# Kernel tuning notes

Measured on AMD Instinct MI355X. Metric: run time of the kernel, lower is better.

## Reference

```python
import jax, jax.numpy as jnp
import numpy as np

EMB = 1024
HEADS = 16
HEAD_DIM = EMB // HEADS
B, S = 4, 2048


def setup_inputs() -> dict:
    key = jax.random.key(0)
    ks = jax.random.split(key, 9)
    sc = 1.0 / np.sqrt(EMB)
    x = jax.random.normal(ks[0], (B, S, EMB), dtype=jnp.float32)
    Wq = jax.random.normal(ks[1], (EMB, EMB), dtype=jnp.float32) * sc
    bq = jax.random.normal(ks[2], (EMB,), dtype=jnp.float32) * 0.02
    Wk = jax.random.normal(ks[3], (EMB, EMB), dtype=jnp.float32) * sc
    bk = jax.random.normal(ks[4], (EMB,), dtype=jnp.float32) * 0.02
    Wv = jax.random.normal(ks[5], (EMB, EMB), dtype=jnp.float32) * sc
    bv = jax.random.normal(ks[6], (EMB,), dtype=jnp.float32) * 0.02
    Wo = jax.random.normal(ks[7], (EMB, EMB), dtype=jnp.float32) * sc
    bo = jax.random.normal(ks[8], (EMB,), dtype=jnp.float32) * 0.02
    # causal mask: 1 where allowed (lower triangular), 0 elsewhere
    causal_mask = jnp.tril(jnp.ones((S, S), dtype=jnp.int32))[None, None]
    return {"x": x, "Wq": Wq, "bq": bq, "Wk": Wk, "bk": bk,
            "Wv": Wv, "bv": bv, "Wo": Wo, "bo": bo,
            "causal_mask": causal_mask}


def reference(x, Wq, bq, Wk, bk, Wv, bv, Wo, bo, causal_mask):
    bs, seq, _ = x.shape
    # nn.Linear: x @ W.T + b; then view [bs, seq, H, hd] and transpose to [bs, H, seq, hd]
    def proj(W, b):
        return (x @ W.T + b).reshape(bs, seq, HEADS, HEAD_DIM).transpose(0, 2, 1, 3)
    q, k, v = proj(Wq, bq), proj(Wk, bk), proj(Wv, bv)
    scale = 1.0 / np.sqrt(HEAD_DIM).astype(np.float32)
    dots = jnp.einsum('bhqd,bhkd->bhqk', q, k) * scale  # [B, H, S, S]
    dots = jnp.where(causal_mask == 0, -jnp.inf, dots)
    attn = jax.nn.softmax(dots, axis=-1)
    out = jnp.einsum('bhqk,bhkd->bhqd', attn, v)  # [B, H, S, hd]
    out = out.transpose(0, 2, 1, 3).reshape(bs, seq, EMB)
    return out @ Wo.T + bo
```

## Files before the change

kernel.cpp:

```cpp
#include <hip/hip_runtime.h>
#include <hip/hip_bf16.h>

typedef __attribute__((ext_vector_type(8))) short short8;
typedef __attribute__((ext_vector_type(4))) float floatx4;

#define B_    4
#define S_    2048
#define EMB_  1024
#define NH_   16
#define HD_   64

#if __has_builtin(__builtin_amdgcn_exp2f)
#define EXP2F(x) __builtin_amdgcn_exp2f(x)
#else
#define EXP2F(x) exp2f(x)
#endif

__device__ __forceinline__ void async_cp16(const void* g, void* l) {
  __builtin_amdgcn_global_load_lds(
      (const __attribute__((address_space(1))) unsigned int*)g,
      (__attribute__((address_space(3))) unsigned int*)l, 16, 0, 0);
}

__device__ __forceinline__ ushort4 cvt4(const float4 f) {
  __bf16 t[4] = {(__bf16)f.x, (__bf16)f.y, (__bf16)f.z, (__bf16)f.w};
  return *(const ushort4*)t;
}

__global__ __launch_bounds__(256)
void cvt_kernel(const float* __restrict__ x,
                const float* __restrict__ wq, const float* __restrict__ wk,
                const float* __restrict__ wv, const float* __restrict__ wo,
                const float* __restrict__ bq, const float* __restrict__ bk,
                const float* __restrict__ bv,
                __bf16* __restrict__ xb, __bf16* __restrict__ Wcat,
                __bf16* __restrict__ Wob, float* __restrict__ bcat)
{
  const int NX4 = 2097152;
  const int NW4 = 262144;
  int g = blockIdx.x * 256 + threadIdx.x;
  if (g < NX4) {
    *(ushort4*)(xb + (size_t)g * 4) = cvt4(*(const float4*)(x + (size_t)g * 4));
    return;
  }
  g -= NX4;
  if (g < 3 * NW4) {
    const float* src = (g < NW4) ? wq : (g < 2 * NW4) ? wk : wv;
    const int gg = (g < NW4) ? g : (g < 2 * NW4) ? g - NW4 : g - 2 * NW4;
    *(ushort4*)(Wcat + (size_t)g * 4) = cvt4(*(const float4*)(src + (size_t)gg * 4));
    return;
  }
  g -= 3 * NW4;
  if (g < NW4) {
    *(ushort4*)(Wob + (size_t)g * 4) = cvt4(*(const float4*)(wo + (size_t)g * 4));
    return;
  }
  g -= NW4;
  if (g < 768) {
    const float* src = (g < 256) ? bq : (g < 512) ? bk : bv;
    *(float4*)(bcat + (size_t)g * 4) = *(const float4*)(src + (size_t)(g & 255) * 4);
  }
}

__global__ __launch_bounds__(256)
void gemm_qkv_kernel(const __bf16* __restrict__ A, const __bf16* __restrict__ W,
                     const float* __restrict__ bcat,
                     __bf16* __restrict__ Qb, __bf16* __restrict__ Kb,
                     __bf16* __restrict__ Vb)
{
  __shared__ __attribute__((aligned(16))) __bf16 As[128 * 32];
  __shared__ __attribute__((aligned(16))) __bf16 Ws[128 * 32];
  const int tid  = threadIdx.x;
  const int wave = tid >> 6, lane = tid & 63;
  const int l15  = lane & 15, quad = lane >> 4;
  const int wm   = wave >> 1, wn = wave & 1;
  const int bm   = blockIdx.y * 128;
  const int bn   = blockIdx.x * 128;
  const int widx = bn >> 10;
  const float QS = 0.180336880f;

  floatx4 acc[4][4];
#pragma unroll
  for (int i = 0; i < 4; ++i)
#pragma unroll
    for (int j = 0; j < 4; ++j) acc[i][j] = (floatx4){0.f, 0.f, 0.f, 0.f};

  const int srow = tid >> 2;
  const int scol = (tid & 3) << 3;
  const __bf16* Ag = A + (size_t)(bm + srow) * 1024 + scol;
  const __bf16* Wg = W + (size_t)(bn + srow) * 1024 + scol;
  __bf16* AsD = As + tid * 8;
  __bf16* WsD = Ws + tid * 8;

  for (int k0 = 0; k0 < 1024; k0 += 32) {
    __syncthreads();
    async_cp16(Ag + k0,             AsD);
    async_cp16(Ag + k0 + 64 * 1024, AsD + 2048);
    async_cp16(Wg + k0,             WsD);
    async_cp16(Wg + k0 + 64 * 1024, WsD + 2048);
    __syncthreads();
    short8 af[4], wf[4];
#pragma unroll
    for (int mi = 0; mi < 4; ++mi)
      af[mi] = *(const short8*)(As + ((wm * 64 + mi * 16 + l15) << 5) + (quad << 3));
#pragma unroll
    for (int ni = 0; ni < 4; ++ni)
      wf[ni] = *(const short8*)(Ws + ((wn * 64 + ni * 16 + l15) << 5) + (quad << 3));
#pragma unroll
    for (int mi = 0; mi < 4; ++mi)
#pragma unroll
      for (int ni = 0; ni < 4; ++ni)
        acc[mi][ni] = __builtin_amdgcn_mfma_f32_16x16x32_bf16(af[mi], wf[ni], acc[mi][ni], 0, 0, 0);
  }

#pragma unroll
  for (int ni = 0; ni < 4; ++ni) {
    const int n  = bn + wn * 64 + ni * 16 + l15;
    const float bvb = bcat[n];
    const int np = n & 1023;
    const int h = np >> 6, d = np & 63;
#pragma unroll
    for (int mi = 0; mi < 4; ++mi) {
      const int m0 = bm + wm * 64 + mi * 16 + quad * 4;
      const int b = m0 >> 11, s0 = m0 & 2047;
      floatx4 v = acc[mi][ni];
      if (widx == 0) {
        const size_t base = (size_t)(b * 16 + h) * (S_ * 64) + d;
#pragma unroll
        for (int r = 0; r < 4; ++r)
          Qb[base + (size_t)(s0 + r) * 64] = (__bf16)((v[r] + bvb) * QS);
      } else if (widx == 1) {
        const size_t base = (size_t)(b * 16 + h) * (S_ * 64) + d;
#pragma unroll
        for (int r = 0; r < 4; ++r)
          Kb[base + (size_t)(s0 + r) * 64] = (__bf16)(v[r] + bvb);
      } else {
        const size_t base = ((size_t)(b * 16 + h) * 64 + d) * S_ + s0;
        union { ushort4 u4; unsigned short u[4]; } pk;
#pragma unroll
        for (int r = 0; r < 4; ++r) {
          __bf16 hv = (__bf16)(v[r] + bvb);
          pk.u[r] = *(unsigned short*)&hv;
        }
        *(ushort4*)(Vb + base) = pk.u4;
      }
    }
  }
}

__device__ __forceinline__ void softmax_update(
    floatx4* s, float& mrun, float& lsum, floatx4* oacc,
    __bf16* psbase, const int l15, const int quad)
{
  float t0 = fmaxf(fmaxf(s[0][0], s[0][1]), fmaxf(s[0][2], s[0][3]));
  float t1 = fmaxf(fmaxf(s[1][0], s[1][1]), fmaxf(s[1][2], s[1][3]));
  float t2 = fmaxf(fmaxf(s[2][0], s[2][1]), fmaxf(s[2][2], s[2][3]));
  float t3 = fmaxf(fmaxf(s[3][0], s[3][1]), fmaxf(s[3][2], s[3][3]));
  float tmax = fmaxf(fmaxf(t0, t1), fmaxf(t2, t3));
  tmax = fmaxf(tmax, __shfl_xor(tmax, 16));
  tmax = fmaxf(tmax, __shfl_xor(tmax, 32));

  const float mold = mrun;
  if (!__all(tmax <= mold + 8.0f)) {
    const float mnew = fmaxf(mold, tmax);
    const float alpha = EXP2F(mold - mnew);
#pragma unroll
    for (int ni = 0; ni < 4; ++ni)
#pragma unroll
      for (int r = 0; r < 4; ++r) oacc[ni][r] *= alpha;
    lsum *= alpha;
    mrun = mnew;
  }
  const float m = mrun;
  float psum = 0.f;
#pragma unroll
  for (int ni = 0; ni < 4; ++ni) {
    float4 p;
    p.x = EXP2F(s[ni][0] - m);
    p.y = EXP2F(s[ni][1] - m);
    p.z = EXP2F(s[ni][2] - m);
    p.w = EXP2F(s[ni][3] - m);
    psum += (p.x + p.y) + (p.z + p.w);
    *(ushort4*)(psbase + l15 * 72 + ni * 16 + quad * 4) = cvt4(p);
  }
  lsum += psum;
}

__global__ __launch_bounds__(256, 3)
void attn_kernel(__bf16* __restrict__ Q, const __bf16* __restrict__ K,
                 const __bf16* __restrict__ Vt)
{
  __shared__ __attribute__((aligned(16))) __bf16 Ks[64 * 72];
  __shared__ __attribute__((aligned(16))) __bf16 Vs[64 * 72];
  __shared__ __attribute__((aligned(16))) __bf16 Ps[4][2][16 * 72];

  const int tid  = threadIdx.x;
  const int wave = tid >> 6, lane = tid & 63;
  const int l15  = lane & 15, quad = lane >> 4;
  const int qtA  = blockIdx.x, bh = blockIdx.y;
  const size_t hb = (size_t)bh * (S_ * 64);
  const float MASKV = -1.0e30f;

  const int srow = tid >> 3;
  const int scol = (tid & 7) << 3;

  const int qtS = qtA;
  const int qtB = 31 - qtA;
  const int myqS = qtS * 64 + wave * 16 + l15;
  const int myqB = qtB * 64 + wave * 16 + l15;

  short8 aqS[2], aqB[2];
#pragma unroll
  for (int kk = 0; kk < 2; ++kk) {
    aqS[kk] = *(const short8*)(Q + hb + (size_t)myqS * 64 + kk * 32 + quad * 8);
    aqB[kk] = *(const short8*)(Q + hb + (size_t)myqB * 64 + kk * 32 + quad * 8);
  }

  floatx4 oaccS[4], oaccB[4];
#pragma unroll
  for (int j = 0; j < 4; ++j) {
    oaccS[j] = (floatx4){0.f, 0.f, 0.f, 0.f};
    oaccB[j] = (floatx4){0.f, 0.f, 0.f, 0.f};
  }
  float lsumS = 0.f, lsumB = 0.f;
  float mrunS = MASKV, mrunB = MASKV;

  uint4 kreg0, kreg1, vreg0, vreg1;
  {
    const __bf16* kp = K  + hb + (size_t)srow * 64 + scol;
    const __bf16* vp = Vt + hb + (size_t)srow * S_ + scol;
    kreg0 = *(const uint4*)kp;
    kreg1 = *(const uint4*)(kp + 32 * 64);
    vreg0 = *(const uint4*)vp;
    vreg1 = *(const uint4*)(vp + (size_t)32 * S_);
  }

  for (int kt = 0; kt <= qtB; ++kt) {
    const bool haveS = (kt <= qtS);

    __syncthreads();
    *(uint4*)(&Ks[srow * 72 + scol])        = kreg0;
    *(uint4*)(&Ks[(srow + 32) * 72 + scol]) = kreg1;
    *(uint4*)(&Vs[srow * 72 + scol])        = vreg0;
    *(uint4*)(&Vs[(srow + 32) * 72 + scol]) = vreg1;
    __syncthreads();

    if (kt < qtB) {
      const __bf16* kp = K  + hb + (size_t)((kt + 1) * 64 + srow) * 64 + scol;
      const __bf16* vp = Vt + hb + (size_t)srow * S_ + (kt + 1) * 64 + scol;
      kreg0 = *(const uint4*)kp;
      kreg1 = *(const uint4*)(kp + 32 * 64);
      vreg0 = *(const uint4*)vp;
      vreg1 = *(const uint4*)(vp + (size_t)32 * S_);
    }

    floatx4 sS[4], sB[4];
#pragma unroll
    for (int j = 0; j < 4; ++j) {
      sS[j] = (floatx4){0.f, 0.f, 0.f, 0.f};
      sB[j] = (floatx4){0.f, 0.f, 0.f, 0.f};
    }
#pragma unroll
    for (int kk = 0; kk < 2; ++kk) {
      short8 bk[4];
#pragma unroll
      for (int ni = 0; ni < 4; ++ni)
        bk[ni] = *(const short8*)(&Ks[(ni * 16 + l15) * 72 + kk * 32 + quad * 8]);
#pragma unroll
      for (int ni = 0; ni < 4; ++ni)
        sB[ni] = __builtin_amdgcn_mfma_f32_16x16x32_bf16(bk[ni], aqB[kk], sB[ni], 0, 0, 0);
      if (haveS) {
#pragma unroll
        for (int ni = 0; ni < 4; ++ni)
          sS[ni] = __builtin_amdgcn_mfma_f32_16x16x32_bf16(bk[ni], aqS[kk], sS[ni], 0, 0, 0);
      }
    }

    if (kt == qtB) {
      const int kb = kt * 64 + quad * 4;
#pragma unroll
      for (int ni = 0; ni < 4; ++ni)
#pragma unroll
        for (int r = 0; r < 4; ++r)
          if (kb + ni * 16 + r > myqB) sB[ni][r] = MASKV;
    }
    if (haveS) {
      if (kt == qtS) {
        const int kb = kt * 64 + quad * 4;
#pragma unroll
        for (int ni = 0; ni < 4; ++ni)
#pragma unroll
          for (int r = 0; r < 4; ++r)
            if (kb + ni * 16 + r > myqS) sS[ni][r] = MASKV;
      }
      softmax_update(sS, mrunS, lsumS, oaccS, &Ps[wave][0][0], l15, quad);
    }
    softmax_update(sB, mrunB, lsumB, oaccB, &Ps[wave][1][0], l15, quad);

    asm volatile("s_waitcnt lgkmcnt(0)" ::: "memory");
    __builtin_amdgcn_sched_barrier(0);

#pragma unroll
    for (int kk = 0; kk < 2; ++kk) {
      short8 bv[4];
#pragma unroll
      for (int ni = 0; ni < 4; ++ni)
        bv[ni] = *(const short8*)(&Vs[(ni * 16 + l15) * 72 + kk * 32 + quad * 8]);
      const short8 pfB = *(const short8*)(&Ps[wave][1][l15 * 72 + kk * 32 + quad * 8]);
#pragma unroll
      for (int ni = 0; ni < 4; ++ni)
        oaccB[ni] = __builtin_amdgcn_mfma_f32_16x16x32_bf16(bv[ni], pfB, oaccB[ni], 0, 0, 0);
      if (haveS) {
        const short8 pfS = *(const short8*)(&Ps[wave][0][l15 * 72 + kk * 32 + quad * 8]);
#pragma unroll
        for (int ni = 0; ni < 4; ++ni)
          oaccS[ni] = __builtin_amdgcn_mfma_f32_16x16x32_bf16(bv[ni], pfS, oaccS[ni], 0, 0, 0);
      }
    }
  }

  {
    float l = lsumS;
    l += __shfl_xor(l, 16);
    l += __shfl_xor(l, 32);
    const float inv = 1.0f / fmaxf(l, 1e-20f);
    const size_t rowb = hb + (size_t)myqS * 64;
#pragma unroll
    for (int ni = 0; ni < 4; ++ni) {
      float4 o;
      o.x = oaccS[ni][0] * inv;
      o.y = oaccS[ni][1] * inv;
      o.z = oaccS[ni][2] * inv;
      o.w = oaccS[ni][3] * inv;
      *(ushort4*)(Q + rowb + ni * 16 + quad * 4) = cvt4(o);
    }
  }
  {
    float l = lsumB;
    l += __shfl_xor(l, 16);
    l += __shfl_xor(l, 32);
    const float inv = 1.0f / fmaxf(l, 1e-20f);
    const size_t rowb = hb + (size_t)myqB * 64;
#pragma unroll
    for (int ni = 0; ni < 4; ++ni) {
      float4 o;
      o.x = oaccB[ni][0] * inv;
      o.y = oaccB[ni][1] * inv;
      o.z = oaccB[ni][2] * inv;
      o.w = oaccB[ni][3] * inv;
      *(ushort4*)(Q + rowb + ni * 16 + quad * 4) = cvt4(o);
    }
  }
}

__global__ __launch_bounds__(256)
void gemm_o_kernel(const __bf16* __restrict__ A, const __bf16* __restrict__ W,
                   const float* __restrict__ bias, float* __restrict__ out)
{
  __shared__ __attribute__((aligned(16))) __bf16 As[128 * 32];
  __shared__ __attribute__((aligned(16))) __bf16 Ws[128 * 32];
  const int tid  = threadIdx.x;
  const int wave = tid >> 6, lane = tid & 63;
  const int l15  = lane & 15, quad = lane >> 4;
  const int wm   = wave >> 1, wn = wave & 1;
  const int bm   = blockIdx.y * 128;
  const int bn   = blockIdx.x * 128;

  floatx4 acc[4][4];
#pragma unroll
  for (int i = 0; i < 4; ++i)
#pragma unroll
    for (int j = 0; j < 4; ++j) acc[i][j] = (floatx4){0.f, 0.f, 0.f, 0.f};

  const int srow = tid >> 2;
  const int scol = (tid & 3) << 3;
  const __bf16* Wg = W + (size_t)(bn + srow) * 1024 + scol;
  const int bb = bm >> 11;
  const int ss = (bm & 2047) + srow;
  __bf16* AsD = As + tid * 8;
  __bf16* WsD = Ws + tid * 8;

  for (int k0 = 0; k0 < 1024; k0 += 32) {
    const int c = k0 + scol, h = c >> 6, dd = c & 63;
    const __bf16* pa0 = A + (((size_t)(bb * 16 + h) * S_) + ss) * 64 + dd;
    __syncthreads();
    async_cp16(pa0,           AsD);
    async_cp16(pa0 + 64 * 64, AsD + 2048);
    async_cp16(Wg + k0,             WsD);
    async_cp16(Wg + k0 + 64 * 1024, WsD + 2048);
    __syncthreads();

    short8 af[4], wf[4];
#pragma unroll
    for (int mi = 0; mi < 4; ++mi)
      af[mi] = *(const short8*)(As + ((wm * 64 + mi * 16 + l15) << 5) + (quad << 3));
#pragma unroll
    for (int ni = 0; ni < 4; ++ni)
      wf[ni] = *(const short8*)(Ws + ((wn * 64 + ni * 16 + l15) << 5) + (quad << 3));
#pragma unroll
    for (int mi = 0; mi < 4; ++mi)
#pragma unroll
      for (int ni = 0; ni < 4; ++ni)
        acc[mi][ni] = __builtin_amdgcn_mfma_f32_16x16x32_bf16(af[mi], wf[ni], acc[mi][ni], 0, 0, 0);
  }

#pragma unroll
  for (int ni = 0; ni < 4; ++ni) {
    const int n = bn + wn * 64 + ni * 16 + l15;
    const float bvb = bias[n];
#pragma unroll
    for (int mi = 0; mi < 4; ++mi) {
      const int m0 = bm + wm * 64 + mi * 16 + quad * 4;
      floatx4 v = acc[mi][ni];
#pragma unroll
      for (int r = 0; r < 4; ++r)
        out[(size_t)(m0 + r) * 1024 + n] = v[r] + bvb;
    }
  }
}

extern "C" void kernel_launch(void* const* d_in, const int* in_sizes, int n_in,
                              void* d_out, int out_size, void* d_ws, size_t ws_size,
                              hipStream_t stream) {
  const float* x  = (const float*)d_in[0];
  const float* Wq = (const float*)d_in[1];
  const float* bq = (const float*)d_in[2];
  const float* Wk = (const float*)d_in[3];
  const float* bk = (const float*)d_in[4];
  const float* Wv = (const float*)d_in[5];
  const float* bv = (const float*)d_in[6];
  const float* Wo = (const float*)d_in[7];
  const float* bo = (const float*)d_in[8];

  const size_t BUF = (size_t)B_ * NH_ * S_ * HD_;
  __bf16* ws   = (__bf16*)d_ws;
  __bf16* xb   = ws;
  __bf16* Wcat = ws + 8388608;
  __bf16* Wob  = ws + 11534336;
  __bf16* Qb   = ws + 12582912;
  float*  bcat = (float*)(ws + 20971520);
  __bf16* Kb   = (__bf16*)d_out;
  __bf16* Vb   = (__bf16*)d_out + BUF;

  dim3 blk(256);
  cvt_kernel<<<12291, blk, 0, stream>>>(x, Wq, Wk, Wv, Wo, bq, bk, bv,
                                        xb, Wcat, Wob, bcat);
  gemm_qkv_kernel<<<dim3(24, 64), blk, 0, stream>>>(xb, Wcat, bcat, Qb, Kb, Vb);
  attn_kernel<<<dim3(16, 64), blk, 0, stream>>>(Qb, Kb, Vb);
  gemm_o_kernel<<<dim3(8, 64), blk, 0, stream>>>(Qb, Wob, bo, (float*)d_out);
}
```

Baseline: 287.2 us.

## Use 128-row query tiles per block with two 16-row groups per wave

Each attention block now handles a 128-row query tile: every wave owns 32 query rows, split into two 16-row sub-blocks, and each K/V tile loaded into LDS is reused for twice as many queries. Causal load balancing pairs tile qtA with tile 15-qtA, which are processed one after the other instead of together. The grid is halved to 8x64 blocks and the occupancy hint drops from 3 to 2 blocks per CU. The aim is to cut K/V global loads and LDS staging per query. In exchange the kernel has fewer blocks, lower occupancy and more registers per wave, and each pair of tiles now runs sequentially with its own K/V loop.

Result: faster. 274.9 us (-4.3%).

```diff
diff --git a/kernel.cpp b/kernel.cpp
--- a/kernel.cpp
+++ b/kernel.cpp
@@ -186,7 +186,7 @@
   lsum += psum;
 }
 
-__global__ __launch_bounds__(256, 3)
+__global__ __launch_bounds__(256, 2)
 void attn_kernel(__bf16* __restrict__ Q, const __bf16* __restrict__ K,
                  const __bf16* __restrict__ Vt)
 {
@@ -204,151 +204,150 @@
   const int srow = tid >> 3;
   const int scol = (tid & 7) << 3;
 
-  const int qtS = qtA;
-  const int qtB = 31 - qtA;
-  const int myqS = qtS * 64 + wave * 16 + l15;
-  const int myqB = qtB * 64 + wave * 16 + l15;
-
-  short8 aqS[2], aqB[2];
-#pragma unroll
-  for (int kk = 0; kk < 2; ++kk) {
-    aqS[kk] = *(const short8*)(Q + hb + (size_t)myqS * 64 + kk * 32 + quad * 8);
-    aqB[kk] = *(const short8*)(Q + hb + (size_t)myqB * 64 + kk * 32 + quad * 8);
-  }
-
-  floatx4 oaccS[4], oaccB[4];
-#pragma unroll
-  for (int j = 0; j < 4; ++j) {
-    oaccS[j] = (floatx4){0.f, 0.f, 0.f, 0.f};
-    oaccB[j] = (floatx4){0.f, 0.f, 0.f, 0.f};
-  }
-  float lsumS = 0.f, lsumB = 0.f;
-  float mrunS = MASKV, mrunB = MASKV;
-
-  uint4 kreg0, kreg1, vreg0, vreg1;
-  {
-    const __bf16* kp = K  + hb + (size_t)srow * 64 + scol;
-    const __bf16* vp = Vt + hb + (size_t)srow * S_ + scol;
-    kreg0 = *(const uint4*)kp;
-    kreg1 = *(const uint4*)(kp + 32 * 64);
-    vreg0 = *(const uint4*)vp;
-    vreg1 = *(const uint4*)(vp + (size_t)32 * S_);
-  }
-
-  for (int kt = 0; kt <= qtB; ++kt) {
-    const bool haveS = (kt <= qtS);
-
-    __syncthreads();
-    *(uint4*)(&Ks[srow * 72 + scol])        = kreg0;
-    *(uint4*)(&Ks[(srow + 32) * 72 + scol]) = kreg1;
-    *(uint4*)(&Vs[srow * 72 + scol])        = vreg0;
-    *(uint4*)(&Vs[(srow + 32) * 72 + scol]) = vreg1;
-    __syncthreads();
-
-    if (kt < qtB) {
-      const __bf16* kp = K  + hb + (size_t)((kt + 1) * 64 + srow) * 64 + scol;
-      const __bf16* vp = Vt + hb + (size_t)srow * S_ + (kt + 1) * 64 + scol;
+  for (int qsel = 0; qsel < 2; ++qsel) {
+    const int qt = qsel ? (15 - qtA) : qtA;
+    const int qw = qt * 128 + wave * 32;
+    const int myqA = qw + l15;
+    const int myqB = qw + 16 + l15;
+    const int nsub = 2 * qt + 2;
+
+    const __bf16* qpA = Q + hb + (size_t)myqA * 64 + quad * 8;
+    const __bf16* qpB = Q + hb + (size_t)myqB * 64 + quad * 8;
+    short8 aqA0 = *(const short8*)(qpA);
+    short8 aqA1 = *(const short8*)(qpA + 32);
+    short8 aqB0 = *(const short8*)(qpB);
+    short8 aqB1 = *(const short8*)(qpB + 32);
+
+    floatx4 oaccA[4], oaccB[4];
+#pragma unroll
+    for (int j = 0; j < 4; ++j) {
+      oaccA[j] = (floatx4){0.f, 0.f, 0.f, 0.f};
+      oaccB[j] = (floatx4){0.f, 0.f, 0.f, 0.f};
+    }
+    float lsumA = 0.f, lsumB = 0.f;
+    float mrunA = MASKV, mrunB = MASKV;
+
+    uint4 kreg0, kreg1, vreg0, vreg1;
+    {
+      const __bf16* kp = K  + hb + (size_t)srow * 64 + scol;
+      const __bf16* vp = Vt + hb + (size_t)srow * S_ + scol;
       kreg0 = *(const uint4*)kp;
       kreg1 = *(const uint4*)(kp + 32 * 64);
       vreg0 = *(const uint4*)vp;
       vreg1 = *(const uint4*)(vp + (size_t)32 * S_);
     }
 
-    floatx4 sS[4], sB[4];
-#pragma unroll
-    for (int j = 0; j < 4; ++j) {
-      sS[j] = (floatx4){0.f, 0.f, 0.f, 0.f};
-      sB[j] = (floatx4){0.f, 0.f, 0.f, 0.f};
-    }
-#pragma unroll
-    for (int kk = 0; kk < 2; ++kk) {
-      short8 bk[4];
-#pragma unroll
-      for (int ni = 0; ni < 4; ++ni)
-        bk[ni] = *(const short8*)(&Ks[(ni * 16 + l15) * 72 + kk * 32 + quad * 8]);
-#pragma unroll
-      for (int ni = 0; ni < 4; ++ni)
-        sB[ni] = __builtin_amdgcn_mfma_f32_16x16x32_bf16(bk[ni], aqB[kk], sB[ni], 0, 0, 0);
-      if (haveS) {
-#pragma unroll
-        for (int ni = 0; ni < 4; ++ni)
-          sS[ni] = __builtin_amdgcn_mfma_f32_16x16x32_bf16(bk[ni], aqS[kk], sS[ni], 0, 0, 0);
+    for (int kt = 0; kt < nsub; ++kt) {
+      __syncthreads();
+      *(uint4*)(&Ks[srow * 72 + scol])        = kreg0;
+      *(uint4*)(&Ks[(srow + 32) * 72 + scol]) = kreg1;
+      *(uint4*)(&Vs[srow * 72 + scol])        = vreg0;
+      *(uint4*)(&Vs[(srow + 32) * 72 + scol]) = vreg1;
+      __syncthreads();
+
+      if (kt + 1 < nsub) {
+        const __bf16* kp = K  + hb + (size_t)((kt + 1) * 64 + srow) * 64 + scol;
+        const __bf16* vp = Vt + hb + (size_t)srow * S_ + (kt + 1) * 64 + scol;
+        kreg0 = *(const uint4*)kp;
+        kreg1 = *(const uint4*)(kp + 32 * 64);
+        vreg0 = *(const uint4*)vp;
+        vreg1 = *(const uint4*)(vp + (size_t)32 * S_);
       }
-    }
-
-    if (kt == qtB) {
-      const int kb = kt * 64 + quad * 4;
-#pragma unroll
-      for (int ni = 0; ni < 4; ++ni)
-#pragma unroll
-        for (int r = 0; r < 4; ++r)
-          if (kb + ni * 16 + r > myqB) sB[ni][r] = MASKV;
-    }
-    if (haveS) {
-      if (kt == qtS) {
+
+      if (kt * 64 <= qw + 31) {
+        floatx4 sA[4], sB[4];
+#pragma unroll
+        for (int j = 0; j < 4; ++j) {
+          sA[j] = (floatx4){0.f, 0.f, 0.f, 0.f};
+          sB[j] = (floatx4){0.f, 0.f, 0.f, 0.f};
+        }
+#pragma unroll
+        for (int kk = 0; kk < 2; ++kk) {
+          const short8 aqa = kk ? aqA1 : aqA0;
+          const short8 aqb = kk ? aqB1 : aqB0;
+          short8 bk[4];
+#pragma unroll
+          for (int ni = 0; ni < 4; ++ni)
+            bk[ni] = *(const short8*)(&Ks[(ni * 16 + l15) * 72 + kk * 32 + quad * 8]);
+#pragma unroll
+          for (int ni = 0; ni < 4; ++ni)
+            sA[ni] = __builtin_amdgcn_mfma_f32_16x16x32_bf16(bk[ni], aqa, sA[ni], 0, 0, 0);
+#pragma unroll
+          for (int ni = 0; ni < 4; ++ni)
+            sB[ni] = __builtin_amdgcn_mfma_f32_16x16x32_bf16(bk[ni], aqb, sB[ni], 0, 0, 0);
+        }
+
         const int kb = kt * 64 + quad * 4;
-#pragma unroll
-        for (int ni = 0; ni < 4; ++ni)
-#pragma unroll
-          for (int r = 0; r < 4; ++r)
-            if (kb + ni * 16 + r > myqS) sS[ni][r] = MASKV;
+        if (kt * 64 + 63 > qw) {
+#pragma unroll
+          for (int ni = 0; ni < 4; ++ni)
+#pragma unroll
+            for (int r = 0; r < 4; ++r)
+              if (kb + ni * 16 + r > myqA) sA[ni][r] = MASKV;
+        }
+        if (kt * 64 + 63 > qw + 16) {
+#pragma unroll
+          for (int ni = 0; ni < 4; ++ni)
+#pragma unroll
+            for (int r = 0; r < 4; ++r)
+              if (kb + ni * 16 + r > myqB) sB[ni][r] = MASKV;
+        }
+
+        softmax_update(sA, mrunA, lsumA, oaccA, &Ps[wave][0][0], l15, quad);
+        softmax_update(sB, mrunB, lsumB, oaccB, &Ps[wave][1][0], l15, quad);
+
+        asm volatile("s_waitcnt lgkmcnt(0)" ::: "memory");
+        __builtin_amdgcn_sched_barrier(0);
+
+#pragma unroll
+        for (int kk = 0; kk < 2; ++kk) {
+          short8 bv[4];
+#pragma unroll
+          for (int ni = 0; ni < 4; ++ni)
+            bv[ni] = *(const short8*)(&Vs[(ni * 16 + l15) * 72 + kk * 32 + quad * 8]);
+          const short8 pfA = *(const short8*)(&Ps[wave][0][l15 * 72 + kk * 32 + quad * 8]);
+          const short8 pfB = *(const short8*)(&Ps[wave][1][l15 * 72 + kk * 32 + quad * 8]);
+#pragma unroll
+          for (int ni = 0; ni < 4; ++ni)
+            oaccA[ni] = __builtin_amdgcn_mfma_f32_16x16x32_bf16(bv[ni], pfA, oaccA[ni], 0, 0, 0);
+#pragma unroll
+          for (int ni = 0; ni < 4; ++ni)
+            oaccB[ni] = __builtin_amdgcn_mfma_f32_16x16x32_bf16(bv[ni], pfB, oaccB[ni], 0, 0, 0);
+        }
       }
-      softmax_update(sS, mrunS, lsumS, oaccS, &Ps[wave][0][0], l15, quad);
-    }
-    softmax_update(sB, mrunB, lsumB, oaccB, &Ps[wave][1][0], l15, quad);
-
-    asm volatile("s_waitcnt lgkmcnt(0)" ::: "memory");
-    __builtin_amdgcn_sched_barrier(0);
-
-#pragma unroll
-    for (int kk = 0; kk < 2; ++kk) {
-      short8 bv[4];
-#pragma unroll
-      for (int ni = 0; ni < 4; ++ni)
-        bv[ni] = *(const short8*)(&Vs[(ni * 16 + l15) * 72 + kk * 32 + quad * 8]);
-      const short8 pfB = *(const short8*)(&Ps[wave][1][l15 * 72 + kk * 32 + quad * 8]);
-#pragma unroll
-      for (int ni = 0; ni < 4; ++ni)
-        oaccB[ni] = __builtin_amdgcn_mfma_f32_16x16x32_bf16(bv[ni], pfB, oaccB[ni], 0, 0, 0);
-      if (haveS) {
-        const short8 pfS = *(const short8*)(&Ps[wave][0][l15 * 72 + kk * 32 + quad * 8]);
-#pragma unroll
-        for (int ni = 0; ni < 4; ++ni)
-          oaccS[ni] = __builtin_amdgcn_mfma_f32_16x16x32_bf16(bv[ni], pfS, oaccS[ni], 0, 0, 0);
+    }
+
+    {
+      float l = lsumA;
+      l += __shfl_xor(l, 16);
+      l += __shfl_xor(l, 32);
+      const float inv = 1.0f / fmaxf(l, 1e-20f);
+      const size_t rowb = hb + (size_t)myqA * 64;
+#pragma unroll
+      for (int ni = 0; ni < 4; ++ni) {
+        float4 o;
+        o.x = oaccA[ni][0] * inv;
+        o.y = oaccA[ni][1] * inv;
+        o.z = oaccA[ni][2] * inv;
+        o.w = oaccA[ni][3] * inv;
+        *(ushort4*)(Q + rowb + ni * 16 + quad * 4) = cvt4(o);
       }
     }
-  }
-
-  {
-    float l = lsumS;
-    l += __shfl_xor(l, 16);
-    l += __shfl_xor(l, 32);
-    const float inv = 1.0f / fmaxf(l, 1e-20f);
-    const size_t rowb = hb + (size_t)myqS * 64;
-#pragma unroll
-    for (int ni = 0; ni < 4; ++ni) {
-      float4 o;
-      o.x = oaccS[ni][0] * inv;
-      o.y = oaccS[ni][1] * inv;
-      o.z = oaccS[ni][2] * inv;
-      o.w = oaccS[ni][3] * inv;
-      *(ushort4*)(Q + rowb + ni * 16 + quad * 4) = cvt4(o);
-    }
-  }
-  {
-    float l = lsumB;
-    l += __shfl_xor(l, 16);
-    l += __shfl_xor(l, 32);
-    const float inv = 1.0f / fmaxf(l, 1e-20f);
-    const size_t rowb = hb + (size_t)myqB * 64;
-#pragma unroll
-    for (int ni = 0; ni < 4; ++ni) {
-      float4 o;
-      o.x = oaccB[ni][0] * inv;
-      o.y = oaccB[ni][1] * inv;
-      o.z = oaccB[ni][2] * inv;
-      o.w = oaccB[ni][3] * inv;
-      *(ushort4*)(Q + rowb + ni * 16 + quad * 4) = cvt4(o);
+    {
+      float l = lsumB;
+      l += __shfl_xor(l, 16);
+      l += __shfl_xor(l, 32);
+      const float inv = 1.0f / fmaxf(l, 1e-20f);
+      const size_t rowb = hb + (size_t)myqB * 64;
+#pragma unroll
+      for (int ni = 0; ni < 4; ++ni) {
+        float4 o;
+        o.x = oaccB[ni][0] * inv;
+        o.y = oaccB[ni][1] * inv;
+        o.z = oaccB[ni][2] * inv;
+        o.w = oaccB[ni][3] * inv;
+        *(ushort4*)(Q + rowb + ni * 16 + quad * 4) = cvt4(o);
+      }
     }
   }
 }
@@ -446,6 +445,6 @@
   cvt_kernel<<<12291, blk, 0, stream>>>(x, Wq, Wk, Wv, Wo, bq, bk, bv,
                                         xb, Wcat, Wob, bcat);
   gemm_qkv_kernel<<<dim3(24, 64), blk, 0, stream>>>(xb, Wcat, bcat, Qb, Kb, Vb);
-  attn_kernel<<<dim3(16, 64), blk, 0, stream>>>(Qb, Kb, Vb);
+  attn_kernel<<<dim3(8, 64), blk, 0, stream>>>(Qb, Kb, Vb);
   gemm_o_kernel<<<dim3(8, 64), blk, 0, stream>>>(Qb, Wob, bo, (float*)d_out);
 }
```
